# Optimization experiments

Measured on AMD Instinct MI355X. Metric: run time of the kernel, lower is better.

The kernel has to match this reference:

```python
import jax, jax.numpy as jnp
import numpy as np
from jax import lax

N, CI, CO, H, W = 2, 256, 256, 64, 64
K, G, DIL, PAD, STRIDE = 3, 8, 1, 1, 1
P = K * K
CG = CO // G  # group channels = 32


def setup_inputs() -> dict:
    key = jax.random.key(0)
    ks = jax.random.split(key, 24)
    r = lambda i, shape, s=1.0: jax.random.normal(ks[i], shape, jnp.float32) * s
    u = lambda i, shape: jax.random.uniform(ks[i], shape, jnp.float32, 0.5, 1.5)
    return dict(
        x=r(0, (N, CI, H, W)),
        conv1_w=r(1, (CO, CI), CI ** -0.5),
        bn1_g=u(2, (CO,)), bn1_b=r(3, (CO,), 0.1), bn1_m=r(4, (CO,), 0.1), bn1_v=u(5, (CO,)),
        inproj_w=r(6, (CO, CO), CO ** -0.5), inproj_b=r(7, (CO,), 0.02),
        dw_w=r(8, (CO, 1, K, K), 0.2), dw_b=r(9, (CO,), 0.02),
        ln_g=u(10, (CO,)), ln_b=r(11, (CO,), 0.02),
        off_w=r(12, (CO, G * P * 2), CO ** -0.5), off_b=jnp.zeros((G * P * 2,), jnp.float32),
        mask_w=r(13, (CO, G * P), CO ** -0.5), mask_b=jnp.zeros((G * P,), jnp.float32),
        outproj_w=r(14, (CO, CO), CO ** -0.5), outproj_b=r(15, (CO,), 0.02),
        bn2_g=u(16, (CO,)), bn2_b=r(17, (CO,), 0.1), bn2_m=r(18, (CO,), 0.1), bn2_v=u(19, (CO,)),
    )


def _bn(x, g, b, m, v, eps):
    # inference-mode BatchNorm2d on NCHW
    return (x - m[:, None, None]) * (g[:, None, None] * lax.rsqrt(v[:, None, None] + eps)) + b[:, None, None]


def _dcn_core(t, offset, mask):
    # t: (N,H,W,C) projected input; offset: (N,H,W,G*P*2); mask: (N,H,W,G,P) softmaxed
    xp = jnp.pad(t, ((0, 0), (PAD, PAD), (PAD, PAD), (0, 0)))
    H_, W_ = H + 2 * PAD, W + 2 * PAD
    # reference points (sample centers), normalized to padded size
    ry = ((DIL * (K - 1)) / 2 + 0.5 + STRIDE * jnp.arange(H, dtype=t.dtype)) / H_
    rx = ((DIL * (K - 1)) / 2 + 0.5 + STRIDE * jnp.arange(W, dtype=t.dtype)) / W_
    base = (DIL * (K - 1)) // 2
    gx = jnp.linspace(-base, -base + (K - 1) * DIL, K, dtype=t.dtype) / W_
    gy = jnp.linspace(-base, -base + (K - 1) * DIL, K, dtype=t.dtype) / H_
    gxx, gyy = jnp.meshgrid(gx, gy, indexing='ij')  # x varies along axis 0 (torch meshgrid order)
    grid = jnp.stack([gxx, gyy], -1).reshape(P, 2)  # (P,2)
    off = offset.reshape(N, H, W, G, P, 2) / jnp.array([W_, H_], t.dtype)
    loc_x = rx[None, None, :, None, None] + grid[:, 0][None, None, None, None] + off[..., 0]  # (N,H,W,G,P)
    loc_y = ry[None, :, None, None, None] + grid[:, 1][None, None, None, None] + off[..., 1]
    # grid_sample(align_corners=False): pixel = norm*size - 0.5
    px = jnp.transpose(loc_x * W_ - 0.5, (0, 3, 1, 2, 4)).reshape(N, G, H * W * P)
    py = jnp.transpose(loc_y * H_ - 0.5, (0, 3, 1, 2, 4)).reshape(N, G, H * W * P)
    # grouped channels-last image: (N,G,H_*W_,CG)
    xg = jnp.transpose(xp.reshape(N, H_, W_, G, CG), (0, 3, 1, 2, 4)).reshape(N, G, H_ * W_, CG)
    x0 = jnp.floor(px)
    y0 = jnp.floor(py)
    wx1 = px - x0
    wy1 = py - y0
    x0i = x0.astype(jnp.int32)
    y0i = y0.astype(jnp.int32)

    def corner(xi, yi, w):
        valid = (xi >= 0) & (xi <= W_ - 1) & (yi >= 0) & (yi <= H_ - 1)
        idx = jnp.clip(yi, 0, H_ - 1) * W_ + jnp.clip(xi, 0, W_ - 1)
        v = jnp.take_along_axis(xg, idx[..., None], axis=2)  # (N,G,M,CG)
        return v * jnp.where(valid, w, 0.0)[..., None]

    sampled = (corner(x0i, y0i, (1 - wx1) * (1 - wy1))
               + corner(x0i + 1, y0i, wx1 * (1 - wy1))
               + corner(x0i, y0i + 1, (1 - wx1) * wy1)
               + corner(x0i + 1, y0i + 1, wx1 * wy1))
    sampled = sampled.reshape(N, G, H * W, P, CG)
    mg = jnp.transpose(mask, (0, 3, 1, 2, 4)).reshape(N, G, H * W, P)
    out = jnp.einsum('nglpc,nglp->nglc', sampled, mg)
    return jnp.transpose(out, (0, 2, 1, 3)).reshape(N, H, W, G * CG)


def reference(x, conv1_w, bn1_g, bn1_b, bn1_m, bn1_v, inproj_w, inproj_b, dw_w, dw_b,
              ln_g, ln_b, off_w, off_b, mask_w, mask_b, outproj_w, outproj_b,
              bn2_g, bn2_b, bn2_m, bn2_v):
    # Conv(inc, ouc, k=1): 1x1 conv (no bias) + BN(eps=1e-3) + SiLU
    y = jnp.einsum('nchw,oc->nohw', x, conv1_w)
    y = jax.nn.silu(_bn(y, bn1_g, bn1_b, bn1_m, bn1_v, 1e-3))
    t = jnp.transpose(y, (0, 2, 3, 1))  # NHWC
    xproj = t @ inproj_w + inproj_b     # input_proj Linear
    # offset/mask branch: depthwise conv (k=3,s=1,p=1) -> LN over C -> GELU
    z = lax.conv_general_dilated(y, dw_w, (1, 1), ((PAD, PAD), (PAD, PAD)),
                                 feature_group_count=CO,
                                 dimension_numbers=('NCHW', 'OIHW', 'NCHW')) + dw_b[None, :, None, None]
    z = jnp.transpose(z, (0, 2, 3, 1))
    mu = jnp.mean(z, -1, keepdims=True)
    var = jnp.var(z, -1, keepdims=True)
    z = (z - mu) * lax.rsqrt(var + 1e-5) * ln_g + ln_b
    z = jax.nn.gelu(z, approximate=False)
    offset = z @ off_w + off_b  # (N,H,W,G*P*2)
    mask = jax.nn.softmax((z @ mask_w + mask_b).reshape(N, H, W, G, P), axis=-1)
    s = _dcn_core(xproj, offset, mask)
    s = s @ outproj_w + outproj_b  # output_proj Linear
    o = jnp.transpose(s, (0, 3, 1, 2))  # back to NCHW
    return jax.nn.silu(_bn(o, bn2_g, bn2_b, bn2_m, bn2_v, 1e-5))
```

## Files before the change

kernel.cpp:

```cpp
#include <hip/hip_runtime.h>
#include <math.h>

#define CC    256
#define HH    64
#define WW    64
#define HWSZ  4096
#define NPIX  8192
#define MT    16
#define ASTR  264

typedef __attribute__((ext_vector_type(8))) short short8;
typedef __attribute__((ext_vector_type(4))) float f32x4;

__device__ __forceinline__ float silu_f(float x) { return x / (1.f + __expf(-x)); }

__device__ __forceinline__ short f2bf(float f) {
    unsigned u = __float_as_uint(f);
    unsigned r = (u + 0x7fffu + ((u >> 16) & 1u)) >> 16;
    return (short)r;
}
__device__ __forceinline__ unsigned pk2(float a, float b) {
    return (unsigned)(unsigned short)f2bf(a) | ((unsigned)(unsigned short)f2bf(b) << 16);
}

__global__ void k_prep(const float* __restrict__ cw, const float* __restrict__ ipw,
                       const float* __restrict__ offw, const float* __restrict__ maskw,
                       const float* __restrict__ opw,
                       const float* __restrict__ offb, const float* __restrict__ maskb,
                       const float* __restrict__ g1, const float* __restrict__ b1,
                       const float* __restrict__ m1, const float* __restrict__ v1,
                       const float* __restrict__ g2, const float* __restrict__ b2,
                       const float* __restrict__ m2, const float* __restrict__ v2,
                       short* __restrict__ Wc1b, short* __restrict__ Wipb,
                       short* __restrict__ Whb, short* __restrict__ Wopb,
                       float* __restrict__ bh, float* __restrict__ sc1, float* __restrict__ sh1,
                       float* __restrict__ sc2, float* __restrict__ sh2) {
    int o = blockIdx.x, c = threadIdx.x;
    Wc1b[o * CC + c] = f2bf(cw[o * CC + c]);
    Wipb[o * CC + c] = f2bf(ipw[c * CC + o]);
    float hv = 0.f;
    if (o < 144) hv = offw[c * 144 + o];
    else if (o < 216) hv = maskw[c * 72 + (o - 144)];
    Whb[o * CC + c] = f2bf(hv);
    Wopb[o * CC + c] = f2bf(opw[c * CC + o]);
    if (o == 0) {
        float bv = 0.f;
        if (c < 144) bv = offb[c];
        else if (c < 216) bv = maskb[c - 144];
        bh[c] = bv;
        float s1 = g1[c] * rsqrtf(v1[c] + 1e-3f);
        sc1[c] = s1; sh1[c] = b1[c] - m1[c] * s1;
        float s2 = g2[c] * rsqrtf(v2[c] + 1e-5f);
        sc2[c] = s2; sh2[c] = b2[c] - m2[c] * s2;
    }
}

__device__ __forceinline__ void prefetch_b(const short* __restrict__ Wb, int lane, int n0,
                                           short8 bf[8][2]) {
    const int m = lane & 15, q = lane >> 4;
#pragma unroll
    for (int kk = 0; kk < 8; ++kk) {
        int c0 = kk * 32 + q * 8;
#pragma unroll
        for (int nt = 0; nt < 2; ++nt)
            bf[kk][nt] = *(const short8*)(Wb + (size_t)(n0 + nt * 16 + m) * CC + c0);
    }
}
__device__ __forceinline__ void mfma_acc(const short* As, const short8 bf[8][2],
                                         int lane, f32x4 acc[2]) {
    const int m = lane & 15, q = lane >> 4;
#pragma unroll
    for (int kk = 0; kk < 8; ++kk) {
        short8 a = *(const short8*)(As + m * ASTR + kk * 32 + q * 8);
#pragma unroll
        for (int nt = 0; nt < 2; ++nt)
            acc[nt] = __builtin_amdgcn_mfma_f32_16x16x32_bf16(a, bf[kk][nt], acc[nt], 0, 0, 0);
    }
}

__global__ __launch_bounds__(512, 4) void k_conv_in(
        const float* __restrict__ x, const short* __restrict__ Wc1b,
        const short* __restrict__ Wipb, const float* __restrict__ sc1,
        const float* __restrict__ sh1, const float* __restrict__ ipb,
        float* __restrict__ y, float* __restrict__ xp) {
    __shared__ __align__(16) short As[MT * ASTR];
    int tid = threadIdx.x, lane = tid & 63, wv = tid >> 6;
    int pix0 = blockIdx.x * MT;
    int n = pix0 >> 12, hw0 = pix0 & (HWSZ - 1);
    int n0 = wv * 32;
    short8 bf[8][2];
    prefetch_b(Wc1b, lane, n0, bf);
    const float* xn = x + (size_t)n * CC * HWSZ;
#pragma unroll
    for (int rep = 0; rep < 2; ++rep) {
        int f = tid + rep * 512;
        int c = f >> 2, i4 = (f & 3) * 4;
        float4 v = *(const float4*)(xn + (size_t)c * HWSZ + hw0 + i4);
        As[(i4 + 0) * ASTR + c] = f2bf(v.x);
        As[(i4 + 1) * ASTR + c] = f2bf(v.y);
        As[(i4 + 2) * ASTR + c] = f2bf(v.z);
        As[(i4 + 3) * ASTR + c] = f2bf(v.w);
    }
    __syncthreads();
    f32x4 acc[2];
    acc[0] = (f32x4){0.f, 0.f, 0.f, 0.f};
    acc[1] = (f32x4){0.f, 0.f, 0.f, 0.f};
    mfma_acc(As, bf, lane, acc);
    __syncthreads();
    prefetch_b(Wipb, lane, n0, bf);
    int col = lane & 15, qr = (lane >> 4) * 4;
#pragma unroll
    for (int nt = 0; nt < 2; ++nt) {
        int o = n0 + nt * 16 + col;
        float sc = sc1[o], sh = sh1[o];
#pragma unroll
        for (int r = 0; r < 4; ++r) {
            int pix = qr + r;
            float val = silu_f(acc[nt][r] * sc + sh);
            y[(size_t)(pix0 + pix) * CC + o] = val;
            As[pix * ASTR + o] = f2bf(val);
        }
    }
    __syncthreads();
    acc[0] = (f32x4){0.f, 0.f, 0.f, 0.f};
    acc[1] = (f32x4){0.f, 0.f, 0.f, 0.f};
    mfma_acc(As, bf, lane, acc);
#pragma unroll
    for (int nt = 0; nt < 2; ++nt) {
        int o = n0 + nt * 16 + col;
        float bo = ipb[o];
#pragma unroll
        for (int r = 0; r < 4; ++r)
            xp[(size_t)(pix0 + qr + r) * CC + o] = acc[nt][r] + bo;
    }
}

__global__ __launch_bounds__(512, 4) void k_tail(
        const float* __restrict__ y, const float* __restrict__ xp,
        const float* __restrict__ dww, const float* __restrict__ dwb,
        const float* __restrict__ lng, const float* __restrict__ lnb,
        const short* __restrict__ Whb, const float* __restrict__ bh,
        const short* __restrict__ Wopb, const float* __restrict__ opb,
        const float* __restrict__ sc2, const float* __restrict__ sh2,
        float* __restrict__ out) {
    __shared__ __align__(16) short As[MT * ASTR];
    __shared__ __align__(16) float buf[4672];
    float* ml   = buf;
    float* loff = buf + 1216;
    float* lm   = buf + 3520;
    float* xs   = buf;

    int tid = threadIdx.x, lane = tid & 63, wv = tid >> 6;
    int pix0 = blockIdx.x * MT;
    int n = pix0 >> 12, hw0 = pix0 & (HWSZ - 1);
    int h = hw0 >> 6, w0 = hw0 & 63;
    int c0 = lane * 4;
    int n0 = wv * 32;
    int col = lane & 15, qr = (lane >> 4) * 4;

    {
        float wloc[36];
        const float4* wp4 = (const float4*)(dww + c0 * 9);
#pragma unroll
        for (int k = 0; k < 9; ++k) ((float4*)wloc)[k] = wp4[k];
        float4 dwbv = *(const float4*)(dwb + c0);
        float4 lngv = *(const float4*)(lng + c0);
        float4 lnbv = *(const float4*)(lnb + c0);
        const float* yn = y + (size_t)n * HWSZ * CC;
#pragma unroll
        for (int i = 0; i < 2; ++i) {
            int pix = wv * 2 + i;
            int w = w0 + pix;
            float4 acc = dwbv;
#pragma unroll
            for (int ky = 0; ky < 3; ++ky) {
                int yy = h + ky - 1;
                if (yy < 0 || yy >= HH) continue;
#pragma unroll
                for (int kx = 0; kx < 3; ++kx) {
                    int xx = w + kx - 1;
                    if (xx < 0 || xx >= WW) continue;
                    float4 yv = *(const float4*)(yn + (size_t)((yy << 6) + xx) * CC + c0);
                    int t = ky * 3 + kx;
                    acc.x += yv.x * wloc[0 * 9 + t];
                    acc.y += yv.y * wloc[1 * 9 + t];
                    acc.z += yv.z * wloc[2 * 9 + t];
                    acc.w += yv.w * wloc[3 * 9 + t];
                }
            }
            float s1 = acc.x + acc.y + acc.z + acc.w;
            float s2 = acc.x * acc.x + acc.y * acc.y + acc.z * acc.z + acc.w * acc.w;
#pragma unroll
            for (int off = 32; off > 0; off >>= 1) {
                s1 += __shfl_xor(s1, off);
                s2 += __shfl_xor(s2, off);
            }
            float mu = s1 * (1.f / 256.f);
            float var = s2 * (1.f / 256.f) - mu * mu;
            float rs = rsqrtf(var + 1e-5f);
            float4 zv;
            zv.x = (acc.x - mu) * rs * lngv.x + lnbv.x;
            zv.y = (acc.y - mu) * rs * lngv.y + lnbv.y;
            zv.z = (acc.z - mu) * rs * lngv.z + lnbv.z;
            zv.w = (acc.w - mu) * rs * lngv.w + lnbv.w;
            zv.x = 0.5f * zv.x * (1.f + erff(zv.x * 0.70710678118654752f));
            zv.y = 0.5f * zv.y * (1.f + erff(zv.y * 0.70710678118654752f));
            zv.z = 0.5f * zv.z * (1.f + erff(zv.z * 0.70710678118654752f));
            zv.w = 0.5f * zv.w * (1.f + erff(zv.w * 0.70710678118654752f));
            *(uint2*)(As + pix * ASTR + c0) = make_uint2(pk2(zv.x, zv.y), pk2(zv.z, zv.w));
        }
    }
    short8 bf[8][2];
    prefetch_b(Whb, lane, n0, bf);
    __syncthreads();

    {
        f32x4 acc[2];
        acc[0] = (f32x4){0.f, 0.f, 0.f, 0.f};
        acc[1] = (f32x4){0.f, 0.f, 0.f, 0.f};
        mfma_acc(As, bf, lane, acc);
#pragma unroll
        for (int nt = 0; nt < 2; ++nt) {
            int o = n0 + nt * 16 + col;
            float bo = bh[o];
#pragma unroll
            for (int r = 0; r < 4; ++r) {
                float v = acc[nt][r] + bo;
                int pix = qr + r;
                if (o < 144) loff[pix * 144 + o] = v;
                else if (o < 216) ml[pix * 76 + (o - 144)] = v;
            }
        }
    }
    __syncthreads();

    if (tid < 128) {
        int pi = tid >> 3, g = tid & 7;
        const float* row = ml + pi * 76 + g * 9;
        float mx = -1e30f;
#pragma unroll
        for (int p = 0; p < 9; ++p) mx = fmaxf(mx, row[p]);
        float e[9], s = 0.f;
#pragma unroll
        for (int p = 0; p < 9; ++p) { e[p] = __expf(row[p] - mx); s += e[p]; }
        float inv = 1.f / s;
        float* mp = lm + pi * 72 + g * 9;
#pragma unroll
        for (int p = 0; p < 9; ++p) mp[p] = e[p] * inv;
    }
    __syncthreads();

    {
        int g = lane >> 3;
        const float* xpn = xp + (size_t)n * HWSZ * CC;
#pragma unroll
        for (int i = 0; i < 2; ++i) {
            int pix = wv * 2 + i;
            int w = w0 + pix;
            float4 acc = make_float4(0.f, 0.f, 0.f, 0.f);
#pragma unroll
            for (int p = 0; p < 9; ++p) {
                float ox = loff[pix * 144 + (g * 9 + p) * 2];
                float oy = loff[pix * 144 + (g * 9 + p) * 2 + 1];
                float px = (float)(w + p / 3) + ox;
                float py = (float)(h + p % 3) + oy;
                float fx = floorf(px), fy = floorf(py);
                float wx1 = px - fx, wy1 = py - fy;
                int x0 = (int)fx, y0 = (int)fy;
                int x1 = x0 + 1, y1 = y0 + 1;
                float mval = lm[pix * 72 + g * 9 + p];
                float w00 = (1.f - wx1) * (1.f - wy1) * mval;
                float w10 = wx1 * (1.f - wy1) * mval;
                float w01 = (1.f - wx1) * wy1 * mval;
                float w11 = wx1 * wy1 * mval;
                if (x0 >= 1 && x0 <= WW && y0 >= 1 && y0 <= HH) {
                    float4 s = *(const float4*)(xpn + (size_t)(((y0 - 1) << 6) + (x0 - 1)) * CC + c0);
                    acc.x += w00 * s.x; acc.y += w00 * s.y; acc.z += w00 * s.z; acc.w += w00 * s.w;
                }
                if (x1 >= 1 && x1 <= WW && y0 >= 1 && y0 <= HH) {
                    float4 s = *(const float4*)(xpn + (size_t)(((y0 - 1) << 6) + (x1 - 1)) * CC + c0);
                    acc.x += w10 * s.x; acc.y += w10 * s.y; acc.z += w10 * s.z; acc.w += w10 * s.w;
                }
                if (x0 >= 1 && x0 <= WW && y1 >= 1 && y1 <= HH) {
                    float4 s = *(const float4*)(xpn + (size_t)(((y1 - 1) << 6) + (x0 - 1)) * CC + c0);
                    acc.x += w01 * s.x; acc.y += w01 * s.y; acc.z += w01 * s.z; acc.w += w01 * s.w;
                }
                if (x1 >= 1 && x1 <= WW && y1 >= 1 && y1 <= HH) {
                    float4 s = *(const float4*)(xpn + (size_t)(((y1 - 1) << 6) + (x1 - 1)) * CC + c0);
                    acc.x += w11 * s.x; acc.y += w11 * s.y; acc.z += w11 * s.z; acc.w += w11 * s.w;
                }
            }
            *(uint2*)(As + pix * ASTR + c0) = make_uint2(pk2(acc.x, acc.y), pk2(acc.z, acc.w));
        }
    }
    prefetch_b(Wopb, lane, n0, bf);
    __syncthreads();

    {
        f32x4 acc[2];
        acc[0] = (f32x4){0.f, 0.f, 0.f, 0.f};
        acc[1] = (f32x4){0.f, 0.f, 0.f, 0.f};
        mfma_acc(As, bf, lane, acc);
#pragma unroll
        for (int nt = 0; nt < 2; ++nt) {
            int o = n0 + nt * 16 + col;
            float bo = opb[o], sc = sc2[o], sh = sh2[o];
#pragma unroll
            for (int r = 0; r < 4; ++r)
                xs[(qr + r) * 260 + o] = silu_f((acc[nt][r] + bo) * sc + sh);
        }
    }
    __syncthreads();

    {
        int i4 = (tid & 3) * 4;
        int obase = tid >> 2;
        float* on = out + (size_t)n * CC * HWSZ + hw0 + i4;
#pragma unroll
        for (int pass = 0; pass < 2; ++pass) {
            int o = obase + pass * 128;
            float4 ov;
            ov.x = xs[(i4 + 0) * 260 + o];
            ov.y = xs[(i4 + 1) * 260 + o];
            ov.z = xs[(i4 + 2) * 260 + o];
            ov.w = xs[(i4 + 3) * 260 + o];
            *(float4*)(on + (size_t)o * HWSZ) = ov;
        }
    }
}

extern "C" void kernel_launch(void* const* d_in, const int* in_sizes, int n_in,
                              void* d_out, int out_size, void* d_ws, size_t ws_size,
                              hipStream_t stream) {
    const float* x        = (const float*)d_in[0];
    const float* conv1_w  = (const float*)d_in[1];
    const float* bn1_g    = (const float*)d_in[2];
    const float* bn1_b    = (const float*)d_in[3];
    const float* bn1_m    = (const float*)d_in[4];
    const float* bn1_v    = (const float*)d_in[5];
    const float* inproj_w = (const float*)d_in[6];
    const float* inproj_b = (const float*)d_in[7];
    const float* dw_w     = (const float*)d_in[8];
    const float* dw_b     = (const float*)d_in[9];
    const float* ln_g     = (const float*)d_in[10];
    const float* ln_b     = (const float*)d_in[11];
    const float* off_w    = (const float*)d_in[12];
    const float* off_b    = (const float*)d_in[13];
    const float* mask_w   = (const float*)d_in[14];
    const float* mask_b   = (const float*)d_in[15];
    const float* outproj_w = (const float*)d_in[16];
    const float* outproj_b = (const float*)d_in[17];
    const float* bn2_g    = (const float*)d_in[18];
    const float* bn2_b    = (const float*)d_in[19];
    const float* bn2_m    = (const float*)d_in[20];
    const float* bn2_v    = (const float*)d_in[21];
    float* out = (float*)d_out;

    short* Wc1b = (short*)d_ws;
    short* Wipb = Wc1b + 65536;
    short* Whb  = Wipb + 65536;
    short* Wopb = Whb + 65536;
    float* fp   = (float*)(Wopb + 65536);
    float* bh   = fp;
    float* sc1  = bh + 256;
    float* sh1  = sc1 + 256;
    float* sc2  = sh1 + 256;
    float* sh2  = sc2 + 256;
    float* y    = sh2 + 256;
    float* xp   = y + 2097152;

    k_prep<<<dim3(CC), dim3(CC), 0, stream>>>(conv1_w, inproj_w, off_w, mask_w, outproj_w,
                                              off_b, mask_b, bn1_g, bn1_b, bn1_m, bn1_v,
                                              bn2_g, bn2_b, bn2_m, bn2_v,
                                              Wc1b, Wipb, Whb, Wopb, bh, sc1, sh1, sc2, sh2);
    k_conv_in<<<dim3(NPIX / MT), dim3(512), 0, stream>>>(x, Wc1b, Wipb, sc1, sh1, inproj_b, y, xp);
    k_tail<<<dim3(NPIX / MT), dim3(512), 0, stream>>>(y, xp, dw_w, dw_b, ln_g, ln_b,
                                                      Whb, bh, Wopb, outproj_b, sc2, sh2, out);
}
```

Before: 166.9 us.

## Store projected input as bf16, shrink tail tile to 8 pixels, branchless gathers

The input-projection output is now written as bf16 and the deformable bilinear gather reads 8-byte bf16 vectors, halving the gather traffic. The tail kernel handles 8 pixels per block (one per wave) with launch bounds raised to 6, which doubles the grid and cuts register and shared-memory use. The mask softmax is folded into each gather thread, the depthwise and bilinear boundary checks become clamped addresses with zero weights, and the output store goes straight from the MFMA accumulators. Weight fragments are loaded inside the GEMM loop instead of being prefetched into registers. In exchange, the 16-row MFMA tile is half empty, xproj loses precision, and out-of-bounds taps now cost loads.

After: 177.2 us. 6.2% more time.

```diff
diff --git a/kernel.cpp b/kernel.cpp
--- a/kernel.cpp
+++ b/kernel.cpp
@@ -7,6 +7,7 @@
 #define HWSZ  4096
 #define NPIX  8192
 #define MT    16
+#define TT    8
 #define ASTR  264
 
 typedef __attribute__((ext_vector_type(8))) short short8;
@@ -21,6 +22,14 @@
 }
 __device__ __forceinline__ unsigned pk2(float a, float b) {
     return (unsigned)(unsigned short)f2bf(a) | ((unsigned)(unsigned short)f2bf(b) << 16);
+}
+__device__ __forceinline__ float4 bf4(uint2 u) {
+    float4 r;
+    r.x = __uint_as_float(u.x << 16);
+    r.y = __uint_as_float(u.x & 0xffff0000u);
+    r.z = __uint_as_float(u.y << 16);
+    r.w = __uint_as_float(u.y & 0xffff0000u);
+    return r;
 }
 
 __global__ void k_prep(const float* __restrict__ cw, const float* __restrict__ ipw,
@@ -55,26 +64,18 @@
     }
 }
 
-__device__ __forceinline__ void prefetch_b(const short* __restrict__ Wb, int lane, int n0,
-                                           short8 bf[8][2]) {
+__device__ __forceinline__ void gemm2(const short* As, const short* __restrict__ Wb,
+                                      int lane, int n0, f32x4 acc[2]) {
     const int m = lane & 15, q = lane >> 4;
 #pragma unroll
     for (int kk = 0; kk < 8; ++kk) {
         int c0 = kk * 32 + q * 8;
-#pragma unroll
-        for (int nt = 0; nt < 2; ++nt)
-            bf[kk][nt] = *(const short8*)(Wb + (size_t)(n0 + nt * 16 + m) * CC + c0);
-    }
-}
-__device__ __forceinline__ void mfma_acc(const short* As, const short8 bf[8][2],
-                                         int lane, f32x4 acc[2]) {
-    const int m = lane & 15, q = lane >> 4;
-#pragma unroll
-    for (int kk = 0; kk < 8; ++kk) {
-        short8 a = *(const short8*)(As + m * ASTR + kk * 32 + q * 8);
-#pragma unroll
-        for (int nt = 0; nt < 2; ++nt)
-            acc[nt] = __builtin_amdgcn_mfma_f32_16x16x32_bf16(a, bf[kk][nt], acc[nt], 0, 0, 0);
+        short8 a = *(const short8*)(As + m * ASTR + c0);
+#pragma unroll
+        for (int nt = 0; nt < 2; ++nt) {
+            short8 b = *(const short8*)(Wb + (size_t)(n0 + nt * 16 + m) * CC + c0);
+            acc[nt] = __builtin_amdgcn_mfma_f32_16x16x32_bf16(a, b, acc[nt], 0, 0, 0);
+        }
     }
 }
 
@@ -82,14 +83,12 @@
         const float* __restrict__ x, const short* __restrict__ Wc1b,
         const short* __restrict__ Wipb, const float* __restrict__ sc1,
         const float* __restrict__ sh1, const float* __restrict__ ipb,
-        float* __restrict__ y, float* __restrict__ xp) {
+        float* __restrict__ y, short* __restrict__ xpb) {
     __shared__ __align__(16) short As[MT * ASTR];
     int tid = threadIdx.x, lane = tid & 63, wv = tid >> 6;
     int pix0 = blockIdx.x * MT;
     int n = pix0 >> 12, hw0 = pix0 & (HWSZ - 1);
     int n0 = wv * 32;
-    short8 bf[8][2];
-    prefetch_b(Wc1b, lane, n0, bf);
     const float* xn = x + (size_t)n * CC * HWSZ;
 #pragma unroll
     for (int rep = 0; rep < 2; ++rep) {
@@ -105,9 +104,8 @@
     f32x4 acc[2];
     acc[0] = (f32x4){0.f, 0.f, 0.f, 0.f};
     acc[1] = (f32x4){0.f, 0.f, 0.f, 0.f};
-    mfma_acc(As, bf, lane, acc);
-    __syncthreads();
-    prefetch_b(Wipb, lane, n0, bf);
+    gemm2(As, Wc1b, lane, n0, acc);
+    __syncthreads();
     int col = lane & 15, qr = (lane >> 4) * 4;
 #pragma unroll
     for (int nt = 0; nt < 2; ++nt) {
@@ -124,34 +122,31 @@
     __syncthreads();
     acc[0] = (f32x4){0.f, 0.f, 0.f, 0.f};
     acc[1] = (f32x4){0.f, 0.f, 0.f, 0.f};
-    mfma_acc(As, bf, lane, acc);
+    gemm2(As, Wipb, lane, n0, acc);
 #pragma unroll
     for (int nt = 0; nt < 2; ++nt) {
         int o = n0 + nt * 16 + col;
         float bo = ipb[o];
 #pragma unroll
         for (int r = 0; r < 4; ++r)
-            xp[(size_t)(pix0 + qr + r) * CC + o] = acc[nt][r] + bo;
-    }
-}
-
-__global__ __launch_bounds__(512, 4) void k_tail(
-        const float* __restrict__ y, const float* __restrict__ xp,
+            xpb[(size_t)(pix0 + qr + r) * CC + o] = f2bf(acc[nt][r] + bo);
+    }
+}
+
+__global__ __launch_bounds__(512, 6) void k_tail(
+        const float* __restrict__ y, const short* __restrict__ xpb,
         const float* __restrict__ dww, const float* __restrict__ dwb,
         const float* __restrict__ lng, const float* __restrict__ lnb,
         const short* __restrict__ Whb, const float* __restrict__ bh,
         const short* __restrict__ Wopb, const float* __restrict__ opb,
         const float* __restrict__ sc2, const float* __restrict__ sh2,
         float* __restrict__ out) {
-    __shared__ __align__(16) short As[MT * ASTR];
-    __shared__ __align__(16) float buf[4672];
-    float* ml   = buf;
-    float* loff = buf + 1216;
-    float* lm   = buf + 3520;
-    float* xs   = buf;
+    __shared__ __align__(16) short As[16 * ASTR];
+    __shared__ float loff[TT * 144];
+    __shared__ float ml[TT * 76];
 
     int tid = threadIdx.x, lane = tid & 63, wv = tid >> 6;
-    int pix0 = blockIdx.x * MT;
+    int pix0 = blockIdx.x * TT;
     int n = pix0 >> 12, hw0 = pix0 & (HWSZ - 1);
     int h = hw0 >> 6, w0 = hw0 & 63;
     int c0 = lane * 4;
@@ -163,168 +158,144 @@
         const float4* wp4 = (const float4*)(dww + c0 * 9);
 #pragma unroll
         for (int k = 0; k < 9; ++k) ((float4*)wloc)[k] = wp4[k];
-        float4 dwbv = *(const float4*)(dwb + c0);
+        float4 acc = *(const float4*)(dwb + c0);
         float4 lngv = *(const float4*)(lng + c0);
         float4 lnbv = *(const float4*)(lnb + c0);
         const float* yn = y + (size_t)n * HWSZ * CC;
-#pragma unroll
-        for (int i = 0; i < 2; ++i) {
-            int pix = wv * 2 + i;
-            int w = w0 + pix;
-            float4 acc = dwbv;
-#pragma unroll
-            for (int ky = 0; ky < 3; ++ky) {
-                int yy = h + ky - 1;
-                if (yy < 0 || yy >= HH) continue;
-#pragma unroll
-                for (int kx = 0; kx < 3; ++kx) {
-                    int xx = w + kx - 1;
-                    if (xx < 0 || xx >= WW) continue;
-                    float4 yv = *(const float4*)(yn + (size_t)((yy << 6) + xx) * CC + c0);
-                    int t = ky * 3 + kx;
-                    acc.x += yv.x * wloc[0 * 9 + t];
-                    acc.y += yv.y * wloc[1 * 9 + t];
-                    acc.z += yv.z * wloc[2 * 9 + t];
-                    acc.w += yv.w * wloc[3 * 9 + t];
-                }
+        int w = w0 + wv;
+#pragma unroll
+        for (int ky = 0; ky < 3; ++ky) {
+            int yy = h + ky - 1;
+            int yc = min(max(yy, 0), HH - 1);
+            float vy = (yy == yc) ? 1.f : 0.f;
+#pragma unroll
+            for (int kx = 0; kx < 3; ++kx) {
+                int xx = w + kx - 1;
+                int xc = min(max(xx, 0), WW - 1);
+                float vm = vy * ((xx == xc) ? 1.f : 0.f);
+                float4 yv = *(const float4*)(yn + (size_t)((yc << 6) + xc) * CC + c0);
+                int t = ky * 3 + kx;
+                acc.x += yv.x * wloc[0 * 9 + t] * vm;
+                acc.y += yv.y * wloc[1 * 9 + t] * vm;
+                acc.z += yv.z * wloc[2 * 9 + t] * vm;
+                acc.w += yv.w * wloc[3 * 9 + t] * vm;
             }
-            float s1 = acc.x + acc.y + acc.z + acc.w;
-            float s2 = acc.x * acc.x + acc.y * acc.y + acc.z * acc.z + acc.w * acc.w;
-#pragma unroll
-            for (int off = 32; off > 0; off >>= 1) {
-                s1 += __shfl_xor(s1, off);
-                s2 += __shfl_xor(s2, off);
-            }
-            float mu = s1 * (1.f / 256.f);
-            float var = s2 * (1.f / 256.f) - mu * mu;
-            float rs = rsqrtf(var + 1e-5f);
-            float4 zv;
-            zv.x = (acc.x - mu) * rs * lngv.x + lnbv.x;
-            zv.y = (acc.y - mu) * rs * lngv.y + lnbv.y;
-            zv.z = (acc.z - mu) * rs * lngv.z + lnbv.z;
-            zv.w = (acc.w - mu) * rs * lngv.w + lnbv.w;
-            zv.x = 0.5f * zv.x * (1.f + erff(zv.x * 0.70710678118654752f));
-            zv.y = 0.5f * zv.y * (1.f + erff(zv.y * 0.70710678118654752f));
-            zv.z = 0.5f * zv.z * (1.f + erff(zv.z * 0.70710678118654752f));
-            zv.w = 0.5f * zv.w * (1.f + erff(zv.w * 0.70710678118654752f));
-            *(uint2*)(As + pix * ASTR + c0) = make_uint2(pk2(zv.x, zv.y), pk2(zv.z, zv.w));
-        }
-    }
-    short8 bf[8][2];
-    prefetch_b(Whb, lane, n0, bf);
+        }
+        float s1 = acc.x + acc.y + acc.z + acc.w;
+        float s2 = acc.x * acc.x + acc.y * acc.y + acc.z * acc.z + acc.w * acc.w;
+#pragma unroll
+        for (int off = 32; off > 0; off >>= 1) {
+            s1 += __shfl_xor(s1, off);
+            s2 += __shfl_xor(s2, off);
+        }
+        float mu = s1 * (1.f / 256.f);
+        float var = s2 * (1.f / 256.f) - mu * mu;
+        float rs = rsqrtf(var + 1e-5f);
+        float4 zv;
+        zv.x = (acc.x - mu) * rs * lngv.x + lnbv.x;
+        zv.y = (acc.y - mu) * rs * lngv.y + lnbv.y;
+        zv.z = (acc.z - mu) * rs * lngv.z + lnbv.z;
+        zv.w = (acc.w - mu) * rs * lngv.w + lnbv.w;
+        zv.x = 0.5f * zv.x * (1.f + erff(zv.x * 0.70710678118654752f));
+        zv.y = 0.5f * zv.y * (1.f + erff(zv.y * 0.70710678118654752f));
+        zv.z = 0.5f * zv.z * (1.f + erff(zv.z * 0.70710678118654752f));
+        zv.w = 0.5f * zv.w * (1.f + erff(zv.w * 0.70710678118654752f));
+        *(uint2*)(As + wv * ASTR + c0) = make_uint2(pk2(zv.x, zv.y), pk2(zv.z, zv.w));
+    }
     __syncthreads();
 
     {
         f32x4 acc[2];
         acc[0] = (f32x4){0.f, 0.f, 0.f, 0.f};
         acc[1] = (f32x4){0.f, 0.f, 0.f, 0.f};
-        mfma_acc(As, bf, lane, acc);
-#pragma unroll
-        for (int nt = 0; nt < 2; ++nt) {
-            int o = n0 + nt * 16 + col;
-            float bo = bh[o];
-#pragma unroll
-            for (int r = 0; r < 4; ++r) {
-                float v = acc[nt][r] + bo;
-                int pix = qr + r;
-                if (o < 144) loff[pix * 144 + o] = v;
-                else if (o < 216) ml[pix * 76 + (o - 144)] = v;
+        gemm2(As, Whb, lane, n0, acc);
+        if (qr < TT) {
+#pragma unroll
+            for (int nt = 0; nt < 2; ++nt) {
+                int o = n0 + nt * 16 + col;
+                float bo = bh[o];
+#pragma unroll
+                for (int r = 0; r < 4; ++r) {
+                    float v = acc[nt][r] + bo;
+                    int pix = qr + r;
+                    if (o < 144) loff[pix * 144 + o] = v;
+                    else if (o < 216) ml[pix * 76 + (o - 144)] = v;
+                }
             }
         }
-    }
-    __syncthreads();
-
-    if (tid < 128) {
-        int pi = tid >> 3, g = tid & 7;
-        const float* row = ml + pi * 76 + g * 9;
-        float mx = -1e30f;
-#pragma unroll
-        for (int p = 0; p < 9; ++p) mx = fmaxf(mx, row[p]);
-        float e[9], s = 0.f;
-#pragma unroll
-        for (int p = 0; p < 9; ++p) { e[p] = __expf(row[p] - mx); s += e[p]; }
-        float inv = 1.f / s;
-        float* mp = lm + pi * 72 + g * 9;
-#pragma unroll
-        for (int p = 0; p < 9; ++p) mp[p] = e[p] * inv;
     }
     __syncthreads();
 
     {
         int g = lane >> 3;
-        const float* xpn = xp + (size_t)n * HWSZ * CC;
-#pragma unroll
-        for (int i = 0; i < 2; ++i) {
-            int pix = wv * 2 + i;
-            int w = w0 + pix;
-            float4 acc = make_float4(0.f, 0.f, 0.f, 0.f);
-#pragma unroll
-            for (int p = 0; p < 9; ++p) {
-                float ox = loff[pix * 144 + (g * 9 + p) * 2];
-                float oy = loff[pix * 144 + (g * 9 + p) * 2 + 1];
-                float px = (float)(w + p / 3) + ox;
-                float py = (float)(h + p % 3) + oy;
-                float fx = floorf(px), fy = floorf(py);
-                float wx1 = px - fx, wy1 = py - fy;
-                int x0 = (int)fx, y0 = (int)fy;
-                int x1 = x0 + 1, y1 = y0 + 1;
-                float mval = lm[pix * 72 + g * 9 + p];
-                float w00 = (1.f - wx1) * (1.f - wy1) * mval;
-                float w10 = wx1 * (1.f - wy1) * mval;
-                float w01 = (1.f - wx1) * wy1 * mval;
-                float w11 = wx1 * wy1 * mval;
-                if (x0 >= 1 && x0 <= WW && y0 >= 1 && y0 <= HH) {
-                    float4 s = *(const float4*)(xpn + (size_t)(((y0 - 1) << 6) + (x0 - 1)) * CC + c0);
-                    acc.x += w00 * s.x; acc.y += w00 * s.y; acc.z += w00 * s.z; acc.w += w00 * s.w;
-                }
-                if (x1 >= 1 && x1 <= WW && y0 >= 1 && y0 <= HH) {
-                    float4 s = *(const float4*)(xpn + (size_t)(((y0 - 1) << 6) + (x1 - 1)) * CC + c0);
-                    acc.x += w10 * s.x; acc.y += w10 * s.y; acc.z += w10 * s.z; acc.w += w10 * s.w;
-                }
-                if (x0 >= 1 && x0 <= WW && y1 >= 1 && y1 <= HH) {
-                    float4 s = *(const float4*)(xpn + (size_t)(((y1 - 1) << 6) + (x0 - 1)) * CC + c0);
-                    acc.x += w01 * s.x; acc.y += w01 * s.y; acc.z += w01 * s.z; acc.w += w01 * s.w;
-                }
-                if (x1 >= 1 && x1 <= WW && y1 >= 1 && y1 <= HH) {
-                    float4 s = *(const float4*)(xpn + (size_t)(((y1 - 1) << 6) + (x1 - 1)) * CC + c0);
-                    acc.x += w11 * s.x; acc.y += w11 * s.y; acc.z += w11 * s.z; acc.w += w11 * s.w;
-                }
-            }
-            *(uint2*)(As + pix * ASTR + c0) = make_uint2(pk2(acc.x, acc.y), pk2(acc.z, acc.w));
-        }
-    }
-    prefetch_b(Wopb, lane, n0, bf);
+        const short* xpn = xpb + (size_t)n * HWSZ * CC;
+        int pix = wv;
+        int w = w0 + pix;
+        float e9[9];
+        {
+            const float* row = ml + pix * 76 + g * 9;
+            float mx = -1e30f;
+#pragma unroll
+            for (int p = 0; p < 9; ++p) { e9[p] = row[p]; mx = fmaxf(mx, e9[p]); }
+            float ssum = 0.f;
+#pragma unroll
+            for (int p = 0; p < 9; ++p) { e9[p] = __expf(e9[p] - mx); ssum += e9[p]; }
+            float inv = 1.f / ssum;
+#pragma unroll
+            for (int p = 0; p < 9; ++p) e9[p] *= inv;
+        }
+        const float* lp = loff + pix * 144 + g * 18;
+        float4 acc = make_float4(0.f, 0.f, 0.f, 0.f);
+#pragma unroll
+        for (int p = 0; p < 9; ++p) {
+            float ox = lp[p * 2], oy = lp[p * 2 + 1];
+            float px = (float)(w + p / 3) + ox;
+            float py = (float)(h + p % 3) + oy;
+            float fx = floorf(px), fy = floorf(py);
+            float wx1 = px - fx, wy1 = py - fy;
+            int x0 = (int)fx, y0 = (int)fy;
+            int x1 = x0 + 1, y1 = y0 + 1;
+            int xc0 = min(max(x0, 1), WW), xc1 = min(max(x1, 1), WW);
+            int yc0 = min(max(y0, 1), HH), yc1 = min(max(y1, 1), HH);
+            float vx0 = (x0 == xc0) ? 1.f : 0.f, vx1 = (x1 == xc1) ? 1.f : 0.f;
+            float vy0 = (y0 == yc0) ? 1.f : 0.f, vy1 = (y1 == yc1) ? 1.f : 0.f;
+            float mval = e9[p];
+            float w00 = (1.f - wx1) * (1.f - wy1) * mval * vx0 * vy0;
+            float w10 = wx1 * (1.f - wy1) * mval * vx1 * vy0;
+            float w01 = (1.f - wx1) * wy1 * mval * vx0 * vy1;
+            float w11 = wx1 * wy1 * mval * vx1 * vy1;
+            uint2 u00 = *(const uint2*)(xpn + (size_t)(((yc0 - 1) << 6) + (xc0 - 1)) * CC + c0);
+            uint2 u10 = *(const uint2*)(xpn + (size_t)(((yc0 - 1) << 6) + (xc1 - 1)) * CC + c0);
+            uint2 u01 = *(const uint2*)(xpn + (size_t)(((yc1 - 1) << 6) + (xc0 - 1)) * CC + c0);
+            uint2 u11 = *(const uint2*)(xpn + (size_t)(((yc1 - 1) << 6) + (xc1 - 1)) * CC + c0);
+            float4 s00 = bf4(u00), s10 = bf4(u10), s01 = bf4(u01), s11 = bf4(u11);
+            acc.x += w00 * s00.x + w10 * s10.x + w01 * s01.x + w11 * s11.x;
+            acc.y += w00 * s00.y + w10 * s10.y + w01 * s01.y + w11 * s11.y;
+            acc.z += w00 * s00.z + w10 * s10.z + w01 * s01.z + w11 * s11.z;
+            acc.w += w00 * s00.w + w10 * s10.w + w01 * s01.w + w11 * s11.w;
+        }
+        *(uint2*)(As + pix * ASTR + c0) = make_uint2(pk2(acc.x, acc.y), pk2(acc.z, acc.w));
+    }
     __syncthreads();
 
     {
         f32x4 acc[2];
         acc[0] = (f32x4){0.f, 0.f, 0.f, 0.f};
         acc[1] = (f32x4){0.f, 0.f, 0.f, 0.f};
-        mfma_acc(As, bf, lane, acc);
-#pragma unroll
-        for (int nt = 0; nt < 2; ++nt) {
-            int o = n0 + nt * 16 + col;
-            float bo = opb[o], sc = sc2[o], sh = sh2[o];
-#pragma unroll
-            for (int r = 0; r < 4; ++r)
-                xs[(qr + r) * 260 + o] = silu_f((acc[nt][r] + bo) * sc + sh);
-        }
-    }
-    __syncthreads();
-
-    {
-        int i4 = (tid & 3) * 4;
-        int obase = tid >> 2;
-        float* on = out + (size_t)n * CC * HWSZ + hw0 + i4;
-#pragma unroll
-        for (int pass = 0; pass < 2; ++pass) {
-            int o = obase + pass * 128;
-            float4 ov;
-            ov.x = xs[(i4 + 0) * 260 + o];
-            ov.y = xs[(i4 + 1) * 260 + o];
-            ov.z = xs[(i4 + 2) * 260 + o];
-            ov.w = xs[(i4 + 3) * 260 + o];
-            *(float4*)(on + (size_t)o * HWSZ) = ov;
+        gemm2(As, Wopb, lane, n0, acc);
+        if (qr < TT) {
+            float* ob = out + (size_t)n * CC * HWSZ + hw0 + qr;
+#pragma unroll
+            for (int nt = 0; nt < 2; ++nt) {
+                int o = n0 + nt * 16 + col;
+                float bo = opb[o], sc = sc2[o], sh = sh2[o];
+                float4 ov;
+                ov.x = silu_f((acc[nt][0] + bo) * sc + sh);
+                ov.y = silu_f((acc[nt][1] + bo) * sc + sh);
+                ov.z = silu_f((acc[nt][2] + bo) * sc + sh);
+                ov.w = silu_f((acc[nt][3] + bo) * sc + sh);
+                *(float4*)(ob + (size_t)o * HWSZ) = ov;
+            }
         }
     }
 }
@@ -367,13 +338,13 @@
     float* sc2  = sh1 + 256;
     float* sh2  = sc2 + 256;
     float* y    = sh2 + 256;
-    float* xp   = y + 2097152;
+    short* xpb  = (short*)(y + 2097152);
 
     k_prep<<<dim3(CC), dim3(CC), 0, stream>>>(conv1_w, inproj_w, off_w, mask_w, outproj_w,
                                               off_b, mask_b, bn1_g, bn1_b, bn1_m, bn1_v,
                                               bn2_g, bn2_b, bn2_m, bn2_v,
                                               Wc1b, Wipb, Whb, Wopb, bh, sc1, sh1, sc2, sh2);
-    k_conv_in<<<dim3(NPIX / MT), dim3(512), 0, stream>>>(x, Wc1b, Wipb, sc1, sh1, inproj_b, y, xp);
-    k_tail<<<dim3(NPIX / MT), dim3(512), 0, stream>>>(y, xp, dw_w, dw_b, ln_g, ln_b,
+    k_conv_in<<<dim3(NPIX / MT), dim3(512), 0, stream>>>(x, Wc1b, Wipb, sc1, sh1, inproj_b, y, xpb);
+    k_tail<<<dim3(NPIX / TT), dim3(512), 0, stream>>>(y, xpb, dw_w, dw_b, ln_g, ln_b,
                                                       Whb, bh, Wopb, outproj_b, sc2, sh2, out);
 }
```
